# Kernel tuning notes

Hardware: AMD Instinct MI355X
Metric: run time of the kernel (lower is better)

## Reference

```python
import jax, jax.numpy as jnp
import numpy as np

IN_C = 7
LOCAL = (64, 64, 64, 128, 1024)
GLOBAL = (512, 128)  # global_channels[-1]=256 halved in __init__
GROUP_NUM = 4
B, N = 16, 16384


def _w(key, out_c, in_c):
    return jax.random.normal(key, (out_c, in_c), dtype=jnp.float32) / np.sqrt(in_c)


def setup_inputs() -> dict:
    key = jax.random.key(0)
    ks = jax.random.split(key, 32)
    inp = {"points": jax.random.normal(ks[0], (B, IN_C, N), dtype=jnp.float32)}
    # mlp_local: Conv1d(k=1) stack IN_C -> LOCAL
    cin = IN_C
    for i, cout in enumerate(LOCAL):
        inp[f"wl{i}"] = _w(ks[1 + i], cout, cin)
        inp[f"bl{i}"] = jnp.zeros((cout,), jnp.float32)
        cin = cout
    # mlp_global: Linear stack 1024 -> GLOBAL
    cin = LOCAL[-1]
    for i, cout in enumerate(GLOBAL):
        inp[f"wg{i}"] = _w(ks[10 + i], cout, cin)
        inp[f"bg{i}"] = jnp.zeros((cout,), jnp.float32)
        cin = cout
    # mlp_group: Linear stack 4096 -> GLOBAL
    cin = LOCAL[-1] * GROUP_NUM
    for i, cout in enumerate(GLOBAL):
        inp[f"wgr{i}"] = _w(ks[20 + i], cout, cin)
        inp[f"bgr{i}"] = jnp.zeros((cout,), jnp.float32)
        cin = cout
    return inp


def _conv_relu(x, w, b):
    # x: (B, Cin, N), w: (Cout, Cin) -> (B, Cout, N)
    return jax.nn.relu(jnp.einsum('bcn,oc->bon', x, w) + b[None, :, None])


def _lin_relu(x, w, b):
    return jax.nn.relu(x @ w.T + b)


def reference(points, wl0, bl0, wl1, bl1, wl2, bl2, wl3, bl3, wl4, bl4,
              wg0, bg0, wg1, bg1, wgr0, bgr0, wgr1, bgr1):
    group_id = jnp.argmax(points[:, 3:, :], axis=1)  # (B, N) in [0, 4)
    x = points
    for w, b in ((wl0, bl0), (wl1, bl1), (wl2, bl2), (wl3, bl3), (wl4, bl4)):
        x = _conv_relu(x, w, b)
    local_feature = x  # (B, 1024, N)
    global_feature = jnp.max(local_feature, axis=2)      # (B, 1024)
    max_indices = jnp.argmax(local_feature, axis=2)      # (B, 1024)
    output_feature = _lin_relu(_lin_relu(global_feature, wg0, bg0), wg1, bg1)  # (B, 128)
    # group-wise max pooling across the WHOLE batch (matches torch boolean-mask loop)
    feats = local_feature.transpose(0, 2, 1).reshape(-1, local_feature.shape[1])  # (B*N, 1024)
    gcf = jax.ops.segment_max(feats, group_id.reshape(-1), num_segments=GROUP_NUM)  # (4, 1024)
    gcf = jnp.where(jnp.isneginf(gcf), 0.0, gcf)  # empty groups stay zero, as in torch
    group_in = jnp.broadcast_to(gcf.reshape(-1)[None, :], (points.shape[0], GROUP_NUM * local_feature.shape[1]))
    group_output_feature = _lin_relu(_lin_relu(group_in, wgr0, bgr0), wgr1, bgr1)  # (B, 128)
    feature = jnp.concatenate([group_output_feature, output_feature], axis=1)  # (B, 256)
    return feature, max_indices
```

## Files before the change

### kernel.cpp

```cpp
#include <hip/hip_runtime.h>
#include <stdint.h>

typedef unsigned int u32;
typedef unsigned long long u64;
typedef unsigned short u16b;
typedef __attribute__((ext_vector_type(8))) _Float16 half8;
typedef __attribute__((ext_vector_type(4))) float v4f;

constexpr int NP = 16384;
constexpr int B0F = 16896, B1F = 16960, B2F = 17024, B3F = 17088, B4F = 17216;
constexpr int GFO = 18240;
constexpr int GCFO = 34624;
constexpr int OF1O = 38720;
constexpr int GR1O = 46912;
constexpr int FIXED_FLOATS = 47424;
constexpr u32 FIXED_BYTES = FIXED_FLOATS * 4;

__device__ __forceinline__ void split2(float x, u16b& h, u16b& l){
  _Float16 hh = (_Float16)x;
  float r = (x - (float)hh) * 2048.f;
  _Float16 ll = (_Float16)r;
  union { _Float16 f; u16b u; } a, b; a.f = hh; b.f = ll;
  h = a.u; l = b.u;
}

__device__ __forceinline__ int swz(int S){ return S ^ ((S >> 3) & 7); }

__global__ __launch_bounds__(256) void k_prep(
    const float* __restrict__ wl0, const float* __restrict__ wl1, const float* __restrict__ wl2,
    const float* __restrict__ wl3, const float* __restrict__ wl4,
    const float* __restrict__ bl0, const float* __restrict__ bl1, const float* __restrict__ bl2,
    const float* __restrict__ bl3, const float* __restrict__ bl4,
    float* __restrict__ wsf, u32 pmax_off, u32 gmax_off, u32 wb_off, int P, int G)
{
  int tid = blockIdx.x * 256 + threadIdx.x;
  u64* pmax = (u64*)((char*)wsf + pmax_off);
  u32* gmax = (u32*)((char*)wsf + gmax_off);
  if (tid < P * 16384) pmax[tid] = 0ull;
  if (tid < G * 4096)  gmax[tid] = 0u;
  if (tid < 131072){
    int ch = tid >> 7, k = tid & 127;
    float x = wl4[tid];
    u16b h, l; split2(x, h, l);
    int kc = k >> 5, q = (k >> 3) & 3, j = k & 7, nt = ch >> 4;
    u32 base = (u32)kc*32768u + (u32)nt*512u + (u32)(((ch & 15) | (q << 4)) * 8 + j);
    u16b* wb = (u16b*)((char*)wsf + wb_off);
    wb[base] = h; wb[131072u + base] = l;
  }
  if (tid < 4096){
    int o = tid >> 6, c = tid & 63;
    float x = wl1[tid];
    u16b h, l; split2(x, h, l);
    u32 a = (u32)((c>>5)*2048 + (o>>4)*512 + (((o&15) | (((c>>3)&3)<<4)) << 3) + (c&7));
    u16b* p = (u16b*)((char*)wsf + wb_off + 524288u);
    p[a] = h; p[4096u + a] = l;
  }
  if (tid < 4096){
    int o = tid >> 6, c = tid & 63;
    float x = wl2[tid];
    u16b h, l; split2(x, h, l);
    u32 a = (u32)((c>>5)*2048 + (o>>4)*512 + (((o&15) | (((c>>3)&3)<<4)) << 3) + (c&7));
    u16b* p = (u16b*)((char*)wsf + wb_off + 524288u + 16384u);
    p[a] = h; p[4096u + a] = l;
  }
  if (tid < 8192){
    int o = tid >> 6, c = tid & 63;
    float x = wl3[tid];
    u16b h, l; split2(x, h, l);
    u32 a = (u32)((c>>5)*4096 + (o>>4)*512 + (((o&15) | (((c>>3)&3)<<4)) << 3) + (c&7));
    u16b* p = (u16b*)((char*)wsf + wb_off + 524288u + 32768u);
    p[a] = h; p[8192u + a] = l;
  }
  if (tid < 8192){
    int s = tid >> 12, rem = tid & 4095;
    int kc = rem >> 11, r2 = rem & 2047;
    int cb = r2 >> 9, slot = (r2 >> 3) & 63, j = r2 & 7;
    int q = slot >> 4, c = kc*32 + q*8 + j, o = cb*16 + (slot & 15);
    float x = (c < 7) ? wl0[o*7 + c] : 0.f;
    u16b h, l; split2(x, h, l);
    u16b* p = (u16b*)((char*)wsf + wb_off + 524288u + 65536u);
    p[(u32)(kc*2048 + cb*512 + slot*8 + j) + (s ? 4096u : 0u)] = s ? l : h;
  }
  if (tid < 64)   wsf[B0F + tid] = bl0[tid];
  if (tid < 64)   wsf[B1F + tid] = bl1[tid];
  if (tid < 64)   wsf[B2F + tid] = bl2[tid];
  if (tid < 128)  wsf[B3F + tid] = bl3[tid];
  if (tid < 1024) wsf[B4F + tid] = bl4[tid];
}

template<int KC>
__device__ __forceinline__ void layer64(const u16b* Fin, u16b* Fout,
    const u16b* __restrict__ wbL, const float* __restrict__ wsf, int bofs,
    int w, int L, int sigL)
{
  int ch = (w << 4) + (L & 15);
  float bias = wsf[bofs + ch];
  v4f D0[4], D1[4];
  #pragma unroll
  for (int m = 0; m < 4; ++m){
    D0[m][0] = bias; D0[m][1] = bias; D0[m][2] = bias; D0[m][3] = bias;
    D1[m] = (v4f)(0.f);
  }
  #pragma unroll
  for (int kc = 0; kc < KC; ++kc){
    const u16b* wp = wbL + (u32)(kc*2048 + w*512 + L*8);
    half8 b0 = *(const half8*)(wp);
    half8 b1 = *(const half8*)(wp + 4096);
    #pragma unroll
    for (int m = 0; m < 4; ++m){
      const u16b* fa = Fin + (u32)((m*2 + kc)*512 + sigL*8);
      half8 a0 = *(const half8*)(fa);
      half8 a1 = *(const half8*)(fa + 4096);
      D0[m] = __builtin_amdgcn_mfma_f32_16x16x32_f16(a0, b0, D0[m], 0, 0, 0);
      D1[m] = __builtin_amdgcn_mfma_f32_16x16x32_f16(a1, b0, D1[m], 0, 0, 0);
      D1[m] = __builtin_amdgcn_mfma_f32_16x16x32_f16(a0, b1, D1[m], 0, 0, 0);
    }
  }
  int kcO = ch >> 5, q = (ch >> 3) & 3, j = ch & 7;
  int rowb = (L >> 4) << 2;
  #pragma unroll
  for (int m = 0; m < 4; ++m){
    #pragma unroll
    for (int r = 0; r < 4; ++r){
      float v = fmaxf(fmaf(D1[m][r], 0x1p-11f, D0[m][r]), 0.f);
      u16b h, l; split2(v, h, l);
      int Sp = swz((rowb + r) | (q << 4));
      u32 a = (u32)((m*2 + kcO)*512 + Sp*8 + j);
      Fout[a] = h; Fout[4096u + a] = l;
    }
  }
}

__global__ __launch_bounds__(256, 2) void k_main(const float* __restrict__ pts,
    const float* __restrict__ wsf,
    const u16b* __restrict__ wb,  const u16b* __restrict__ wb1,
    const u16b* __restrict__ wb2, const u16b* __restrict__ wb3,
    const u16b* __restrict__ wb0,
    u64* __restrict__ pmax, u32* __restrict__ gmax,
    int pmask, int gmask)
{
  __shared__ __align__(16) float sB[12288];
  u16b* LB = (u16b*)sB;
  u16b* FI = LB + 8192;
  float* A0F = sB + 8192;
  u32* gmL = (u32*)(sB + 8192);
  const int t = threadIdx.x;
  const int b = blockIdx.x >> 8;
  const int tile = blockIdx.x & 255;
  const int n0 = tile * 64;
  const int w = t >> 6;
  const int L = t & 63;
  const int sigL = swz(L);
  const int qb = (L >> 4) << 2;

  u64* gmS = (u64*)(sB + 8640);
  if (t < 4) gmS[t] = 0ull;
  {
    u32* FIz = (u32*)FI;
    for (int e = t; e < 4096; e += 256) FIz[e] = 0u;
  }
  for (int e = t; e < 7*64; e += 256)
    A0F[e] = pts[(b*7 + (e >> 6))*NP + n0 + (e & 63)];
  __syncthreads();

  if (t < 64){
    float v = A0F[3*64 + t]; int gi = 0;
    float u1 = A0F[4*64 + t]; if (u1 > v){ v = u1; gi = 1; }
    float u2 = A0F[5*64 + t]; if (u2 > v){ v = u2; gi = 2; }
    float u3 = A0F[6*64 + t]; if (u3 > v){ v = u3; gi = 3; }
    atomicOr(&gmS[gi], 1ull << t);
  }

  for (int e = t; e < 448; e += 256){
    int k = e >> 6, pt = e & 63;
    u16b h, l; split2(A0F[e], h, l);
    u32 a = (u32)((pt >> 4)*1024 + swz(pt & 15)*8 + k);
    FI[a] = h; FI[4096u + a] = l;
  }
  __syncthreads();

  u32 g1lo = (u32)gmS[1], g1hi = (u32)(gmS[1] >> 32);
  u32 g2lo = (u32)gmS[2], g2hi = (u32)(gmS[2] >> 32);
  u32 g3lo = (u32)gmS[3], g3hi = (u32)(gmS[3] >> 32);
  u32 ggpack = 0;
  #pragma unroll
  for (int i = 0; i < 16; ++i){
    int m = i >> 2, r = i & 3;
    int sh = ((m & 1) << 4) + qb + r;
    u32 b1 = ((m < 2 ? g1lo : g1hi) >> sh) & 1u;
    u32 b2 = ((m < 2 ? g2lo : g2hi) >> sh) & 1u;
    u32 b3 = ((m < 2 ? g3lo : g3hi) >> sh) & 1u;
    u32 g = b1 + (b2 << 1) + (b3 << 1) + b3;
    ggpack |= g << (2*i);
  }

  layer64<1>(FI, LB, wb0, wsf, B0F, w, L, sigL);
  __syncthreads();
  layer64<2>(LB, LB + 8192, wb1, wsf, B1F, w, L, sigL);
  __syncthreads();
  layer64<2>(LB + 8192, LB, wb2, wsf, B2F, w, L, sigL);
  __syncthreads();

  v4f Ef[2][4];
  #pragma unroll
  for (int c = 0; c < 2; ++c){
    int chc = ((w*2 + c) << 4) + (L & 15);
    float biasc = wsf[B3F + chc];
    v4f D0[4], D1[4];
    #pragma unroll
    for (int m = 0; m < 4; ++m){
      D0[m][0] = biasc; D0[m][1] = biasc; D0[m][2] = biasc; D0[m][3] = biasc;
      D1[m] = (v4f)(0.f);
    }
    #pragma unroll
    for (int kc = 0; kc < 2; ++kc){
      const u16b* wp = wb3 + (u32)(kc*4096 + (w*2 + c)*512 + L*8);
      half8 b0 = *(const half8*)(wp);
      half8 b1 = *(const half8*)(wp + 8192);
      #pragma unroll
      for (int m = 0; m < 4; ++m){
        const u16b* fa = LB + (u32)((m*2 + kc)*512 + sigL*8);
        half8 a0 = *(const half8*)(fa);
        half8 a1 = *(const half8*)(fa + 4096);
        D0[m] = __builtin_amdgcn_mfma_f32_16x16x32_f16(a0, b0, D0[m], 0, 0, 0);
        D1[m] = __builtin_amdgcn_mfma_f32_16x16x32_f16(a1, b0, D1[m], 0, 0, 0);
        D1[m] = __builtin_amdgcn_mfma_f32_16x16x32_f16(a0, b1, D1[m], 0, 0, 0);
      }
    }
    #pragma unroll
    for (int m = 0; m < 4; ++m)
      #pragma unroll
      for (int r = 0; r < 4; ++r)
        Ef[c][m][r] = fmaf(D1[m][r], 0x1p-11f, D0[m][r]);
  }
  __syncthreads();

  for (int e = t; e < 4096; e += 256) gmL[e] = 0u;
  #pragma unroll
  for (int c = 0; c < 2; ++c){
    int cb = w*2 + c;
    int ch = (cb << 4) + (L & 15);
    int kc4 = cb >> 1, q = (ch >> 3) & 3, j = ch & 7;
    #pragma unroll
    for (int m = 0; m < 4; ++m){
      #pragma unroll
      for (int r = 0; r < 4; ++r){
        float v = fmaxf(Ef[c][m][r], 0.f);
        u16b h, l; split2(v, h, l);
        int Sp = swz((qb + r) | (q << 4));
        u32 a = (u32)((m*4 + kc4)*512 + Sp*8 + j);
        LB[a] = h; LB[8192u + a] = l;
      }
    }
  }
  __syncthreads();

  u64* pslot = pmax + (size_t)(tile & pmask)*(16*1024) + b*1024;
  u32* gslot = gmax + (size_t)(tile & gmask)*4096;
  const char* wbc = (const char*)wb;
  const u32 bvo = (u32)L * 16u;

  u32 voff[16];
  #pragma unroll
  for (int i = 0; i < 16; ++i)
    voff[i] = (u32)((L & 15) << 4) + (((ggpack >> (2*i)) & 3u) << 2);

  half8 bh0, bl0, bh1, bl1;
  {
    u32 base0 = ((u32)(w << 4)) * 1024u + bvo;
    bh0 = *(const half8*)(wbc +           base0);
    bl0 = *(const half8*)(wbc + 262144u + base0);
    bh1 = *(const half8*)(wbc +           base0 + 1024u);
    bl1 = *(const half8*)(wbc + 262144u + base0 + 1024u);
  }
  for (int nti = 0; nti < 8; ++nti){
    const int nt = (w << 4) + (nti << 1);
    const u32 ch0 = (u32)(nt << 4) + (u32)(L & 15);
    float bias0 = wsf[B4F + ch0];
    float bias1 = wsf[B4F + ch0 + 16];
    v4f D0[2][4], D1[2][4];
    #pragma unroll
    for (int m = 0; m < 4; ++m){
      D0[0][m][0] = bias0; D0[0][m][1] = bias0; D0[0][m][2] = bias0; D0[0][m][3] = bias0;
      D0[1][m][0] = bias1; D0[1][m][1] = bias1; D0[1][m][2] = bias1; D0[1][m][3] = bias1;
      D1[0][m] = (v4f)(0.f); D1[1][m] = (v4f)(0.f);
    }
    #pragma unroll
    for (int kc = 0; kc < 4; ++kc){
      half8 c0h = bh0, c0l = bl0, c1h = bh1, c1l = bl1;
      {
        int knext = (kc == 3) ? 0 : kc + 1;
        int ntn   = (kc == 3) ? nt + 2 : nt;
        u32 bofs = (u32)knext*65536u + (u32)ntn*1024u + bvo;
        bh0 = *(const half8*)(wbc +           bofs);
        bl0 = *(const half8*)(wbc + 262144u + bofs);
        bh1 = *(const half8*)(wbc +           bofs + 1024u);
        bl1 = *(const half8*)(wbc + 262144u + bofs + 1024u);
      }
      #pragma unroll
      for (int m = 0; m < 4; ++m){
        const u16b* fb = LB + (u32)((m*4 + kc)*512 + sigL*8);
        half8 a0 = *(const half8*)(fb);
        half8 a1 = *(const half8*)(fb + 8192);
        D0[0][m] = __builtin_amdgcn_mfma_f32_16x16x32_f16(a0, c0h, D0[0][m], 0, 0, 0);
        D0[1][m] = __builtin_amdgcn_mfma_f32_16x16x32_f16(a0, c1h, D0[1][m], 0, 0, 0);
        D1[0][m] = __builtin_amdgcn_mfma_f32_16x16x32_f16(a1, c0h, D1[0][m], 0, 0, 0);
        D1[1][m] = __builtin_amdgcn_mfma_f32_16x16x32_f16(a1, c1h, D1[1][m], 0, 0, 0);
        D1[0][m] = __builtin_amdgcn_mfma_f32_16x16x32_f16(a0, c0l, D1[0][m], 0, 0, 0);
        D1[1][m] = __builtin_amdgcn_mfma_f32_16x16x32_f16(a0, c1l, D1[1][m], 0, 0, 0);
      }
    }
    #pragma unroll
    for (int p = 0; p < 2; ++p){
      char* gmNT = (char*)gmL + ((nt + p) << 8);
      float mx = 0.f; int mi = 0;
      #pragma unroll
      for (int m = 0; m < 4; ++m){
        #pragma unroll
        for (int r = 0; r < 4; ++r){
          int i = m*4 + r;
          float v = fmaxf(fmaf(D1[p][m][r], 0x1p-11f, D0[p][m][r]), 0.f);
          int pidx = n0 + m*16 + qb + r;
          if (i == 0){ mx = v; mi = pidx; }
          else if (v > mx){ mx = v; mi = pidx; }
          atomicMax((u32*)(gmNT + voff[i]), __float_as_uint(v));
        }
      }
      #pragma unroll
      for (int s = 16; s <= 32; s <<= 1){
        float m2 = __shfl_xor(mx, s);
        int  i2  = __shfl_xor(mi, s);
        if (m2 > mx || (m2 == mx && i2 < mi)){ mx = m2; mi = i2; }
      }
      if (L < 16){
        int ch = ((nt + p) << 4) + L;
        u64 pk = ((u64)__float_as_uint(mx) << 32) | (u64)(0xFFFFFFFFu - (u32)mi);
        atomicMax(pslot + ch, pk);
      }
    }
  }

  __syncthreads();
  for (int e = t; e < 4096; e += 256){
    u32 val = gmL[e];
    if (val) atomicMax(gslot + ((e & 3) << 10) + (e >> 2), val);
  }
}

__global__ __launch_bounds__(256) void k_reduce(float* __restrict__ wsf, float* __restrict__ out,
                                                u32 pmax_off, u32 gmax_off, int P, int G)
{
  int e = blockIdx.x * 256 + threadIdx.x;
  u64* pmax = (u64*)((char*)wsf + pmax_off);
  u32* gmax = (u32*)((char*)wsf + gmax_off);
  if (e < 16384){
    u64 m = 0ull;
    for (int s = 0; s < P; ++s){ u64 v = pmax[s*16384 + e]; if (v > m) m = v; }
    float val = __uint_as_float((u32)(m >> 32));
    u32 idx = 0xFFFFFFFFu - (u32)(m & 0xFFFFFFFFull);
    wsf[GFO + e] = val;
    out[4096 + e] = (float)idx;
  } else if (e < 20480){
    int e2 = e - 16384;
    u32 mg = 0u;
    for (int s = 0; s < G; ++s){ u32 v = gmax[s*4096 + e2]; if (v > mg) mg = v; }
    wsf[GCFO + e2] = __uint_as_float(mg);
  }
}

__global__ __launch_bounds__(256) void k_mlp1(float* __restrict__ wsf,
    const float* __restrict__ wg0, const float* __restrict__ bg0,
    const float* __restrict__ wgr0, const float* __restrict__ bgr0)
{
  int wid = (blockIdx.x * 256 + threadIdx.x) >> 6;
  int lane = threadIdx.x & 63;
  if (wid < 8192){
    int b = wid >> 9, o = wid & 511;
    const float* gf = wsf + GFO + b*1024;
    float s = 0.f;
    #pragma unroll
    for (int i = 0; i < 16; ++i){ int k = lane + (i << 6); s = fmaf(gf[k], wg0[o*1024 + k], s); }
    for (int off = 32; off; off >>= 1) s += __shfl_down(s, off);
    if (lane == 0) wsf[OF1O + b*512 + o] = fmaxf(s + bg0[o], 0.f);
  } else if (wid < 8704){
    int o = wid - 8192;
    const float* gcf = wsf + GCFO;
    float s = 0.f;
    #pragma unroll 8
    for (int i = 0; i < 64; ++i){ int k = lane + (i << 6); s = fmaf(gcf[k], wgr0[o*4096 + k], s); }
    for (int off = 32; off; off >>= 1) s += __shfl_down(s, off);
    if (lane == 0) wsf[GR1O + o] = fmaxf(s + bgr0[o], 0.f);
  }
}

__global__ __launch_bounds__(256) void k_mlp2(const float* __restrict__ wsf,
    const float* __restrict__ wg1, const float* __restrict__ bg1,
    const float* __restrict__ wgr1, const float* __restrict__ bgr1,
    float* __restrict__ out)
{
  int wid = (blockIdx.x * 256 + threadIdx.x) >> 6;
  int lane = threadIdx.x & 63;
  if (wid < 2048){
    int b = wid >> 7, o = wid & 127;
    const float* of1 = wsf + OF1O + b*512;
    float s = 0.f;
    #pragma unroll
    for (int i = 0; i < 8; ++i){ int k = lane + (i << 6); s = fmaf(of1[k], wg1[o*512 + k], s); }
    for (int off = 32; off; off >>= 1) s += __shfl_down(s, off);
    if (lane == 0) out[b*256 + 128 + o] = fmaxf(s + bg1[o], 0.f);
  } else if (wid < 2176){
    int o = wid - 2048;
    const float* gr1 = wsf + GR1O;
    float s = 0.f;
    #pragma unroll
    for (int i = 0; i < 8; ++i){ int k = lane + (i << 6); s = fmaf(gr1[k], wgr1[o*512 + k], s); }
    for (int off = 32; off; off >>= 1) s += __shfl_down(s, off);
    if (lane == 0){
      float r = fmaxf(s + bgr1[o], 0.f);
      for (int bb = 0; bb < 16; ++bb) out[bb*256 + o] = r;
    }
  }
}

extern "C" void kernel_launch(void* const* d_in, const int* in_sizes, int n_in,
                              void* d_out, int out_size, void* d_ws, size_t ws_size,
                              hipStream_t stream)
{
  const float* pts  = (const float*)d_in[0];
  const float* wl0  = (const float*)d_in[1];  const float* bl0 = (const float*)d_in[2];
  const float* wl1  = (const float*)d_in[3];  const float* bl1 = (const float*)d_in[4];
  const float* wl2  = (const float*)d_in[5];  const float* bl2 = (const float*)d_in[6];
  const float* wl3  = (const float*)d_in[7];  const float* bl3 = (const float*)d_in[8];
  const float* wl4  = (const float*)d_in[9];  const float* bl4 = (const float*)d_in[10];
  const float* wg0  = (const float*)d_in[11]; const float* bg0 = (const float*)d_in[12];
  const float* wg1  = (const float*)d_in[13]; const float* bg1 = (const float*)d_in[14];
  const float* wgr0 = (const float*)d_in[15]; const float* bgr0 = (const float*)d_in[16];
  const float* wgr1 = (const float*)d_in[17]; const float* bgr1 = (const float*)d_in[18];
  float* wsf = (float*)d_ws;
  float* out = (float*)d_out;

  int P, G;
  if      (ws_size >= 2400000) { P = 8; G = 16; }
  else if (ws_size >= 1700000) { P = 4; G = 8;  }
  else if (ws_size >= 1360000) { P = 2; G = 4;  }
  else                         { P = 1; G = 2;  }
  u32 pmax_off = FIXED_BYTES;
  u32 gmax_off = pmax_off + (u32)P * 131072u;
  u32 wb_off   = gmax_off + (u32)G * 16384u;
  u32 wb1_off  = wb_off + 524288u;
  u32 wb2_off  = wb1_off + 16384u;
  u32 wb3_off  = wb2_off + 16384u;
  u32 wb0_off  = wb3_off + 32768u;

  k_prep<<<dim3(1024), dim3(256), 0, stream>>>(wl0, wl1, wl2, wl3, wl4,
      bl0, bl1, bl2, bl3, bl4, wsf, pmax_off, gmax_off, wb_off, P, G);
  k_main<<<dim3(4096), dim3(256), 0, stream>>>(pts, wsf,
      (const u16b*)((char*)d_ws + wb_off),  (const u16b*)((char*)d_ws + wb1_off),
      (const u16b*)((char*)d_ws + wb2_off), (const u16b*)((char*)d_ws + wb3_off),
      (const u16b*)((char*)d_ws + wb0_off),
      (u64*)((char*)d_ws + pmax_off), (u32*)((char*)d_ws + gmax_off), P-1, G-1);
  k_reduce<<<dim3(80), dim3(256), 0, stream>>>(wsf, out, pmax_off, gmax_off, P, G);
  k_mlp1<<<dim3(2176), dim3(256), 0, stream>>>(wsf, wg0, bg0, wgr0, bgr0);
  k_mlp2<<<dim3(544), dim3(256), 0, stream>>>(wsf, wg1, bg1, wgr1, bgr1, out);
}
```

Baseline: 347.2 us.

## Fuse partial-max reduction into first MLP kernel and raise MFMA wave priority

Removes the separate k_reduce launch. Each k_mlp1 block now redundantly reduces the per-slot pmax/gmax partials into shared memory, then computes its four output neurons from LDS, and designated blocks write the argmax indices. It also wraps the MFMA inner loops in the main kernel with s_setprio(1)/s_setprio(0) to favour waves issuing matrix ops. This saves one launch and a global round trip, at the cost of repeated partial-max reads across the 128 blocks per batch and 128 group blocks.

```diff
diff --git a/kernel.cpp b/kernel.cpp
--- a/kernel.cpp
+++ b/kernel.cpp
@@ -9,8 +9,6 @@
 
 constexpr int NP = 16384;
 constexpr int B0F = 16896, B1F = 16960, B2F = 17024, B3F = 17088, B4F = 17216;
-constexpr int GFO = 18240;
-constexpr int GCFO = 34624;
 constexpr int OF1O = 38720;
 constexpr int GR1O = 46912;
 constexpr int FIXED_FLOATS = 47424;
@@ -106,6 +104,7 @@
     const u16b* wp = wbL + (u32)(kc*2048 + w*512 + L*8);
     half8 b0 = *(const half8*)(wp);
     half8 b1 = *(const half8*)(wp + 4096);
+    __builtin_amdgcn_s_setprio(1);
     #pragma unroll
     for (int m = 0; m < 4; ++m){
       const u16b* fa = Fin + (u32)((m*2 + kc)*512 + sigL*8);
@@ -115,6 +114,7 @@
       D1[m] = __builtin_amdgcn_mfma_f32_16x16x32_f16(a1, b0, D1[m], 0, 0, 0);
       D1[m] = __builtin_amdgcn_mfma_f32_16x16x32_f16(a0, b1, D1[m], 0, 0, 0);
     }
+    __builtin_amdgcn_s_setprio(0);
   }
   int kcO = ch >> 5, q = (ch >> 3) & 3, j = ch & 7;
   int rowb = (L >> 4) << 2;
@@ -217,6 +217,7 @@
       const u16b* wp = wb3 + (u32)(kc*4096 + (w*2 + c)*512 + L*8);
       half8 b0 = *(const half8*)(wp);
       half8 b1 = *(const half8*)(wp + 8192);
+      __builtin_amdgcn_s_setprio(1);
       #pragma unroll
       for (int m = 0; m < 4; ++m){
         const u16b* fa = LB + (u32)((m*2 + kc)*512 + sigL*8);
@@ -226,6 +227,7 @@
         D1[m] = __builtin_amdgcn_mfma_f32_16x16x32_f16(a1, b0, D1[m], 0, 0, 0);
         D1[m] = __builtin_amdgcn_mfma_f32_16x16x32_f16(a0, b1, D1[m], 0, 0, 0);
       }
+      __builtin_amdgcn_s_setprio(0);
     }
     #pragma unroll
     for (int m = 0; m < 4; ++m)
@@ -297,6 +299,7 @@
         bh1 = *(const half8*)(wbc +           bofs + 1024u);
         bl1 = *(const half8*)(wbc + 262144u + bofs + 1024u);
       }
+      __builtin_amdgcn_s_setprio(1);
       #pragma unroll
       for (int m = 0; m < 4; ++m){
         const u16b* fb = LB + (u32)((m*4 + kc)*512 + sigL*8);
@@ -309,6 +312,7 @@
         D1[0][m] = __builtin_amdgcn_mfma_f32_16x16x32_f16(a0, c0l, D1[0][m], 0, 0, 0);
         D1[1][m] = __builtin_amdgcn_mfma_f32_16x16x32_f16(a0, c1l, D1[1][m], 0, 0, 0);
       }
+      __builtin_amdgcn_s_setprio(0);
     }
     #pragma unroll
     for (int p = 0; p < 2; ++p){
@@ -347,47 +351,48 @@
   }
 }
 
-__global__ __launch_bounds__(256) void k_reduce(float* __restrict__ wsf, float* __restrict__ out,
-                                                u32 pmax_off, u32 gmax_off, int P, int G)
-{
-  int e = blockIdx.x * 256 + threadIdx.x;
+__global__ __launch_bounds__(256) void k_mlp1(float* __restrict__ wsf, float* __restrict__ out,
+    const float* __restrict__ wg0, const float* __restrict__ bg0,
+    const float* __restrict__ wgr0, const float* __restrict__ bgr0,
+    u32 pmax_off, u32 gmax_off, int P, int G)
+{
+  __shared__ float red[4096];
+  const int blk = blockIdx.x;
+  const int tid = threadIdx.x;
+  const int lane = tid & 63;
+  const int wv = tid >> 6;
   u64* pmax = (u64*)((char*)wsf + pmax_off);
   u32* gmax = (u32*)((char*)wsf + gmax_off);
-  if (e < 16384){
-    u64 m = 0ull;
-    for (int s = 0; s < P; ++s){ u64 v = pmax[s*16384 + e]; if (v > m) m = v; }
-    float val = __uint_as_float((u32)(m >> 32));
-    u32 idx = 0xFFFFFFFFu - (u32)(m & 0xFFFFFFFFull);
-    wsf[GFO + e] = val;
-    out[4096 + e] = (float)idx;
-  } else if (e < 20480){
-    int e2 = e - 16384;
-    u32 mg = 0u;
-    for (int s = 0; s < G; ++s){ u32 v = gmax[s*4096 + e2]; if (v > mg) mg = v; }
-    wsf[GCFO + e2] = __uint_as_float(mg);
-  }
-}
-
-__global__ __launch_bounds__(256) void k_mlp1(float* __restrict__ wsf,
-    const float* __restrict__ wg0, const float* __restrict__ bg0,
-    const float* __restrict__ wgr0, const float* __restrict__ bgr0)
-{
-  int wid = (blockIdx.x * 256 + threadIdx.x) >> 6;
-  int lane = threadIdx.x & 63;
-  if (wid < 8192){
-    int b = wid >> 9, o = wid & 511;
-    const float* gf = wsf + GFO + b*1024;
+  if (blk < 2048){
+    int b = blk >> 7;
+    const bool emit = (blk & 127) == 0;
+    for (int e = tid; e < 1024; e += 256){
+      u64 m = 0ull;
+      for (int s = 0; s < P; ++s){ u64 v = pmax[s*16384 + b*1024 + e]; if (v > m) m = v; }
+      red[e] = __uint_as_float((u32)(m >> 32));
+      if (emit){
+        u32 idx = 0xFFFFFFFFu - (u32)(m & 0xFFFFFFFFull);
+        out[4096 + b*1024 + e] = (float)idx;
+      }
+    }
+    __syncthreads();
+    int o = ((blk & 127) << 2) + wv;
     float s = 0.f;
     #pragma unroll
-    for (int i = 0; i < 16; ++i){ int k = lane + (i << 6); s = fmaf(gf[k], wg0[o*1024 + k], s); }
+    for (int i = 0; i < 16; ++i){ int k = lane + (i << 6); s = fmaf(red[k], wg0[o*1024 + k], s); }
     for (int off = 32; off; off >>= 1) s += __shfl_down(s, off);
     if (lane == 0) wsf[OF1O + b*512 + o] = fmaxf(s + bg0[o], 0.f);
-  } else if (wid < 8704){
-    int o = wid - 8192;
-    const float* gcf = wsf + GCFO;
+  } else {
+    for (int e = tid; e < 4096; e += 256){
+      u32 mg = 0u;
+      for (int s2 = 0; s2 < G; ++s2){ u32 v = gmax[s2*4096 + e]; if (v > mg) mg = v; }
+      red[e] = __uint_as_float(mg);
+    }
+    __syncthreads();
+    int o = ((blk - 2048) << 2) + wv;
     float s = 0.f;
     #pragma unroll 8
-    for (int i = 0; i < 64; ++i){ int k = lane + (i << 6); s = fmaf(gcf[k], wgr0[o*4096 + k], s); }
+    for (int i = 0; i < 64; ++i){ int k = lane + (i << 6); s = fmaf(red[k], wgr0[o*4096 + k], s); }
     for (int off = 32; off; off >>= 1) s += __shfl_down(s, off);
     if (lane == 0) wsf[GR1O + o] = fmaxf(s + bgr0[o], 0.f);
   }
@@ -459,7 +464,7 @@
       (const u16b*)((char*)d_ws + wb2_off), (const u16b*)((char*)d_ws + wb3_off),
       (const u16b*)((char*)d_ws + wb0_off),
       (u64*)((char*)d_ws + pmax_off), (u32*)((char*)d_ws + gmax_off), P-1, G-1);
-  k_reduce<<<dim3(80), dim3(256), 0, stream>>>(wsf, out, pmax_off, gmax_off, P, G);
-  k_mlp1<<<dim3(2176), dim3(256), 0, stream>>>(wsf, wg0, bg0, wgr0, bgr0);
+  k_mlp1<<<dim3(2176), dim3(256), 0, stream>>>(wsf, out, wg0, bg0, wgr0, bgr0,
+      pmax_off, gmax_off, P, G);
   k_mlp2<<<dim3(544), dim3(256), 0, stream>>>(wsf, wg1, bg1, wgr1, bgr1, out);
 }
```

Result: slower. 380.1 us (+9.5%).
